# Kernel optimization log

Hardware: AMD Instinct MI355X
Metric: run time of the kernel (lower is better)

## Reference

```python
import jax, jax.numpy as jnp
import numpy as np

HEADS = 8
WSZ = 8
DIM_KEY = 32
DIM_VALUE = 32
DIM = 256
EPS = 1e-5


def setup_inputs() -> dict:
    key = jax.random.key(0)
    ks = jax.random.split(key, 8)
    B, C, H, W = 16, DIM, 128, 128
    inner_k = DIM_KEY * HEADS
    inner_v = DIM_VALUE * HEADS
    x = jax.random.normal(ks[0], (B, C, H, W), dtype=jnp.float32)
    g = jnp.ones((C,), dtype=jnp.float32)
    b = jnp.zeros((C,), dtype=jnp.float32)
    wq = jax.random.normal(ks[1], (inner_k, C), dtype=jnp.float32) * (C ** -0.5)
    wk = jax.random.normal(ks[2], (inner_k, C), dtype=jnp.float32) * (C ** -0.5)
    wv = jax.random.normal(ks[3], (inner_v, C), dtype=jnp.float32) * (C ** -0.5)
    local_w = jax.random.normal(ks[4], (inner_v, inner_v, 3, 3), dtype=jnp.float32) * ((inner_v * 9) ** -0.5)
    local_b = jnp.zeros((inner_v,), dtype=jnp.float32)
    out_w = jax.random.normal(ks[5], (C, inner_v), dtype=jnp.float32) * (inner_v ** -0.5)
    out_b = jnp.zeros((C,), dtype=jnp.float32)
    return {"x": x, "g": g, "b": b, "wq": wq, "wk": wk, "wv": wv,
            "local_w": local_w, "local_b": local_b, "out_w": out_w, "out_b": out_b}


def _to_windows(t, heads, wsz):
    # [B, heads*d, H, W] -> [B*X*Y, heads, wsz*wsz, d]
    B, Ch, H, W = t.shape
    d = Ch // heads
    X, Y = H // wsz, W // wsz
    t = t.reshape(B, heads, d, X, wsz, Y, wsz)
    t = t.transpose(0, 3, 5, 1, 4, 6, 2)  # B X Y heads w1 w2 d
    return t.reshape(B * X * Y, heads, wsz * wsz, d)


def _from_windows(t, B, heads, wsz, H, W):
    X, Y = H // wsz, W // wsz
    d = t.shape[-1]
    t = t.reshape(B, X, Y, heads, wsz, wsz, d)
    t = t.transpose(0, 3, 6, 1, 4, 2, 5)  # B heads d X w1 Y w2
    return t.reshape(B, heads * d, H, W)


def reference(x, g, b, wq, wk, wv, local_w, local_b, out_w, out_b):
    B, C, H, W = x.shape
    # ChanLayerNorm over channel dim (biased var)
    mean = jnp.mean(x, axis=1, keepdims=True)
    var = jnp.var(x, axis=1, keepdims=True)
    xn = (x - mean) / jnp.sqrt(var + EPS) * g[None, :, None, None] + b[None, :, None, None]
    # 1x1 conv projections as einsum
    q = jnp.einsum('oc,bchw->bohw', wq, xn)
    k = jnp.einsum('oc,bchw->bohw', wk, xn)
    v = jnp.einsum('oc,bchw->bohw', wv, xn)
    # local interactive 3x3 conv on v
    local_out = jax.lax.conv_general_dilated(
        v, local_w, window_strides=(1, 1), padding='SAME',
        dimension_numbers=('NCHW', 'OIHW', 'NCHW')) + local_b[None, :, None, None]
    # windowed attention
    qw = _to_windows(q, HEADS, WSZ)
    kw = _to_windows(k, HEADS, WSZ)
    vw = _to_windows(v, HEADS, WSZ)
    scale = DIM_KEY ** -0.5
    dots = jnp.einsum('whid,whjd->whij', qw, kw) * scale
    attn = jax.nn.softmax(dots, axis=-1)
    out = jnp.einsum('whij,whjd->whid', attn, vw)
    out = _from_windows(out, B, HEADS, WSZ, H, W)
    out = out + local_out
    # to_out 1x1 conv with bias
    return jnp.einsum('oc,bchw->bohw', out_w, out) + out_b[None, :, None, None]
```

## Files before the change

kernel.cpp:

```cpp
#include <hip/hip_runtime.h>

typedef __attribute__((ext_vector_type(8))) short short8;
typedef __attribute__((ext_vector_type(4))) float f32x4;
typedef __attribute__((ext_vector_type(2))) _Float16 h2;
typedef __attribute__((ext_vector_type(8))) _Float16 h8;

#define DEV static __device__ __forceinline__

typedef __attribute__((address_space(1))) void GVoid;
typedef __attribute__((address_space(3))) void LVoid;

DEV unsigned short f2h(float f) {
  _Float16 h = (_Float16)f;
  return __builtin_bit_cast(unsigned short, h);
}
DEV float h2f(unsigned short u) {
  return (float)__builtin_bit_cast(_Float16, u);
}
DEV unsigned pkh(float a, float b) {
  h2 h;
  h.x = (_Float16)a;
  h.y = (_Float16)b;
  return __builtin_bit_cast(unsigned, h);
}
DEV void cp16(void* lds_uniform_base, const void* gsrc) {
  __builtin_amdgcn_global_load_lds((GVoid*)gsrc, (LVoid*)lds_uniform_base, 16, 0, 0);
}
DEV float fdot2(h2 a, h2 b, float c) {
  return __builtin_amdgcn_fdot2(a, b, c, false);
}

DEV void xcd_remap(int& mb, int& nb) {
  const int gx = gridDim.x;
  const int p = blockIdx.x + gx * blockIdx.y;
  const int nwg = gx * gridDim.y;
  const int q = nwg >> 3;
  const int L = (p & 7) * q + (p >> 3);
  mb = L % gx;
  nb = L / gx;
}

__global__ __launch_bounds__(256) void setup_kernel(
    const float* __restrict__ wq, const float* __restrict__ wk, const float* __restrict__ wv,
    const float* __restrict__ lw, const float* __restrict__ ow,
    unsigned short* __restrict__ wqkvb, unsigned short* __restrict__ w2b,
    unsigned short* __restrict__ woutb, unsigned short* __restrict__ zp)
{
  int i = blockIdx.x * 256 + threadIdx.x;
  if (i < 196608) {
    float f = (i < 65536) ? wq[i] : (i < 131072) ? wk[i - 65536] : wv[i - 131072];
    wqkvb[i] = f2h(f);
  } else if (i < 786432) {
    int j = i - 196608;
    int co = j / 2304;
    int r = j - co * 2304;
    int tap = r >> 8;
    int ci = r & 255;
    w2b[j] = f2h(lw[(co * 256 + ci) * 9 + tap]);
  } else if (i < 851968) {
    int j = i - 786432;
    woutb[j] = f2h(ow[j]);
  } else if (i < 852096) {
    zp[i - 851968] = 0;
  }
}

__global__ __launch_bounds__(256) void ln_kernel(
    const float* __restrict__ x, const float* __restrict__ gw,
    const float* __restrict__ bw, unsigned short* __restrict__ xn)
{
  const int t = threadIdx.x;
  const int p = blockIdx.x * 256 + t;
  const int b = p >> 14;
  const int pix = p & 16383;
  const int h = pix >> 7;
  const int w = pix & 127;
  const float* xp = x + ((size_t)b << 22) + pix;

  float sum = 0.f, ss = 0.f;
#pragma unroll 8
  for (int c = 0; c < 256; ++c) {
    float f = xp[(size_t)c << 14];
    sum += f;
    ss += f * f;
  }
  float mean = sum * (1.f / 256.f);
  float var = ss * (1.f / 256.f) - mean * mean;
  float inv = rsqrtf(var + 1e-5f);

  const int pw = ((b * 16 + (h >> 3)) * 16 + (w >> 3)) * 64 + (h & 7) * 8 + (w & 7);
  unsigned short* op = xn + (size_t)pw * 256;
#pragma unroll 2
  for (int c = 0; c < 256; c += 4) {
    float f0 = xp[(size_t)(c + 0) << 14];
    float f1 = xp[(size_t)(c + 1) << 14];
    float f2 = xp[(size_t)(c + 2) << 14];
    float f3 = xp[(size_t)(c + 3) << 14];
    float v0 = (f0 - mean) * inv * gw[c + 0] + bw[c + 0];
    float v1 = (f1 - mean) * inv * gw[c + 1] + bw[c + 1];
    float v2 = (f2 - mean) * inv * gw[c + 2] + bw[c + 2];
    float v3 = (f3 - mean) * inv * gw[c + 3] + bw[c + 3];
    unsigned long long pk = (unsigned long long)pkh(v0, v1) |
                            ((unsigned long long)pkh(v2, v3) << 32);
    *(unsigned long long*)(op + c) = pk;
  }
}

DEV void mfma_tile(const unsigned short* As, const unsigned short* Bs,
                   int wm, int wn, int l15, int quad, f32x4 (&acc)[4][4])
{
  const int sx = l15 & 7;
#pragma unroll
  for (int ks = 0; ks < 2; ++ks) {
    const int sl = ((ks * 4 + quad) ^ sx) * 8;
    short8 a[4], b[4];
#pragma unroll
    for (int i = 0; i < 4; ++i)
      a[i] = *(const short8*)(As + (wm + i * 16 + l15) * 64 + sl);
#pragma unroll
    for (int j = 0; j < 4; ++j)
      b[j] = *(const short8*)(Bs + (wn + j * 16 + l15) * 64 + sl);
#pragma unroll
    for (int i = 0; i < 4; ++i)
#pragma unroll
      for (int j = 0; j < 4; ++j)
        acc[i][j] = __builtin_amdgcn_mfma_f32_16x16x32_f16(
            __builtin_bit_cast(h8, a[i]), __builtin_bit_cast(h8, b[j]), acc[i][j], 0, 0, 0);
  }
}

__global__ __launch_bounds__(256) void qkv_gemm(
    const unsigned short* __restrict__ wqkvb, const unsigned short* __restrict__ xn,
    unsigned short* __restrict__ qb, unsigned short* __restrict__ kb,
    unsigned short* __restrict__ vb)
{
  __shared__ __align__(16) unsigned short As[128 * 64];
  __shared__ __align__(16) unsigned short Bs[128 * 64];
  const int tid = threadIdx.x;
  const int lane = tid & 63;
  const int wave = tid >> 6;
  const int l15 = lane & 15;
  const int quad = lane >> 4;
  const int wm = (wave >> 1) * 64;
  const int wn = (wave & 1) * 64;
  const int sub = tid & 7;
  const int row0 = tid >> 3;
  const int ssub = sub ^ (row0 & 7);
  int mb, nb;
  xcd_remap(mb, nb);
  const int m0 = mb * 128;
  const int n0 = nb * 128;

  f32x4 acc[4][4];
  f32x4 zero = {0.f, 0.f, 0.f, 0.f};
#pragma unroll
  for (int i = 0; i < 4; ++i)
#pragma unroll
    for (int j = 0; j < 4; ++j) acc[i][j] = zero;

  for (int kt = 0; kt < 4; ++kt) {
    const int k0 = kt * 64;
#pragma unroll
    for (int it = 0; it < 4; ++it) {
      const int row = it * 32 + row0;
      cp16(As + (size_t)(it * 256 + wave * 64) * 8,
           wqkvb + (size_t)(m0 + row) * 256 + k0 + ssub * 8);
      cp16(Bs + (size_t)(it * 256 + wave * 64) * 8,
           xn + (size_t)(n0 + row) * 256 + k0 + ssub * 8);
    }
    __syncthreads();
    mfma_tile(As, Bs, wm, wn, l15, quad, acc);
    __syncthreads();
  }

  unsigned short* ob = (m0 < 256) ? qb : (m0 < 512) ? kb : vb;
  const int chb = (m0 & 255) + wm;
#pragma unroll
  for (int i = 0; i < 4; ++i) {
    const int ch = chb + i * 16 + quad * 4;
#pragma unroll
    for (int j = 0; j < 4; ++j) {
      const int n = n0 + wn + j * 16 + l15;
      unsigned long long pk = (unsigned long long)pkh(acc[i][j][0], acc[i][j][1]) |
                              ((unsigned long long)pkh(acc[i][j][2], acc[i][j][3]) << 32);
      *(unsigned long long*)(ob + (size_t)n * 256 + ch) = pk;
    }
  }
}

__global__ __launch_bounds__(128) void attn_kernel(
    const unsigned short* __restrict__ qb, const unsigned short* __restrict__ kb,
    const unsigned short* __restrict__ vb, unsigned short* __restrict__ attnb)
{
  __shared__ __align__(16) _Float16 ks2[2][64][40];
  __shared__ __align__(16) _Float16 vs2[2][32][64];
  const int tid = threadIdx.x;
  const int tok = tid & 63;
  const int hs = tid >> 6;
  const int win = blockIdx.x >> 2;
  const int head = (blockIdx.x & 3) * 2 + hs;
  const size_t base = (size_t)(win * 64 + tok) * 256 + head * 32;

  h2 q2[16];
  {
    const uint4* qp4 = (const uint4*)(qb + base);
    const uint4* kp4 = (const uint4*)(kb + base);
    const uint4* vp4 = (const uint4*)(vb + base);
    const _Float16 sc = (_Float16)0.17677669529663688f;
    h2 sc2;
    sc2.x = sc;
    sc2.y = sc;
#pragma unroll
    for (int i = 0; i < 4; ++i) {
      uint4 u = qp4[i];
      q2[i * 4 + 0] = __builtin_bit_cast(h2, u.x) * sc2;
      q2[i * 4 + 1] = __builtin_bit_cast(h2, u.y) * sc2;
      q2[i * 4 + 2] = __builtin_bit_cast(h2, u.z) * sc2;
      q2[i * 4 + 3] = __builtin_bit_cast(h2, u.w) * sc2;
      *(uint4*)&ks2[hs][tok][8 * i] = kp4[i];
      uint4 v = vp4[i];
      unsigned vv[4] = {v.x, v.y, v.z, v.w};
#pragma unroll
      for (int w = 0; w < 4; ++w) {
        h2 hv = __builtin_bit_cast(h2, vv[w]);
        int c = 2 * (i * 4 + w);
        vs2[hs][c + 0][tok] = hv.x;
        vs2[hs][c + 1][tok] = hv.y;
      }
    }
  }
  __syncthreads();

  float dots[64];
#pragma unroll
  for (int j = 0; j < 64; ++j) {
    const uint4* kr = (const uint4*)ks2[hs][j];
    float d = 0.f;
#pragma unroll
    for (int qq = 0; qq < 4; ++qq) {
      uint4 raw = kr[qq];
      d = fdot2(q2[4 * qq + 0], __builtin_bit_cast(h2, raw.x), d);
      d = fdot2(q2[4 * qq + 1], __builtin_bit_cast(h2, raw.y), d);
      d = fdot2(q2[4 * qq + 2], __builtin_bit_cast(h2, raw.z), d);
      d = fdot2(q2[4 * qq + 3], __builtin_bit_cast(h2, raw.w), d);
    }
    dots[j] = d;
  }
  float mx = -1e30f;
#pragma unroll
  for (int j = 0; j < 64; ++j) mx = fmaxf(mx, dots[j]);
  float s = 0.f;
#pragma unroll
  for (int j = 0; j < 64; ++j) {
    float e = __expf(dots[j] - mx);
    dots[j] = e;
    s += e;
  }
  const float rs = 1.f / s;

  h2 p2[32];
#pragma unroll
  for (int jp = 0; jp < 32; ++jp) {
    h2 p;
    p.x = (_Float16)dots[2 * jp];
    p.y = (_Float16)dots[2 * jp + 1];
    p2[jp] = p;
  }

  float of[32];
#pragma unroll
  for (int c = 0; c < 32; ++c) {
    const uint4* vr = (const uint4*)vs2[hs][c];
    float o = 0.f;
#pragma unroll
    for (int qq = 0; qq < 8; ++qq) {
      uint4 raw = vr[qq];
      o = fdot2(p2[4 * qq + 0], __builtin_bit_cast(h2, raw.x), o);
      o = fdot2(p2[4 * qq + 1], __builtin_bit_cast(h2, raw.y), o);
      o = fdot2(p2[4 * qq + 2], __builtin_bit_cast(h2, raw.z), o);
      o = fdot2(p2[4 * qq + 3], __builtin_bit_cast(h2, raw.w), o);
    }
    of[c] = o;
  }

  uint4* op4 = (uint4*)(attnb + base);
#pragma unroll
  for (int i = 0; i < 4; ++i) {
    uint4 o;
    o.x = pkh(of[8 * i + 0] * rs, of[8 * i + 1] * rs);
    o.y = pkh(of[8 * i + 2] * rs, of[8 * i + 3] * rs);
    o.z = pkh(of[8 * i + 4] * rs, of[8 * i + 5] * rs);
    o.w = pkh(of[8 * i + 6] * rs, of[8 * i + 7] * rs);
    op4[i] = o;
  }
}

__global__ __launch_bounds__(256) void conv_gemm(
    const unsigned short* __restrict__ w2b, const unsigned short* __restrict__ vbuf,
    const unsigned short* __restrict__ attnb, const float* __restrict__ lbias,
    const unsigned short* __restrict__ zp, unsigned short* __restrict__ sumb)
{
  __shared__ __align__(16) unsigned short As[128 * 64];
  __shared__ __align__(16) unsigned short Bs[128 * 64];
  const int tid = threadIdx.x;
  const int lane = tid & 63;
  const int wave = tid >> 6;
  const int l15 = lane & 15;
  const int quad = lane >> 4;
  const int wm = (wave >> 1) * 64;
  const int wn = (wave & 1) * 64;
  const int sub = tid & 7;
  const int row0 = tid >> 3;
  const int ssub = sub ^ (row0 & 7);
  int mb, nb;
  xcd_remap(mb, nb);
  const int m0 = mb * 128;
  const int n0 = nb * 128;

  int bi[4], hh[4], ww[4];
#pragma unroll
  for (int it = 0; it < 4; ++it) {
    int n = n0 + it * 32 + row0;
    int b = n >> 14;
    int r = n & 16383;
    int Xw = r >> 10;
    int r2 = r & 1023;
    int Yw = r2 >> 6;
    int t2 = r2 & 63;
    bi[it] = b;
    hh[it] = Xw * 8 + (t2 >> 3);
    ww[it] = Yw * 8 + (t2 & 7);
  }

  f32x4 acc[4][4];
  f32x4 zero = {0.f, 0.f, 0.f, 0.f};
#pragma unroll
  for (int i = 0; i < 4; ++i)
#pragma unroll
    for (int j = 0; j < 4; ++j) acc[i][j] = zero;

  for (int tap = 0; tap < 9; ++tap) {
    const int dy = tap / 3 - 1;
    const int dx = tap - (tap / 3) * 3 - 1;
    const unsigned short* bp[4];
    int bstep[4];
#pragma unroll
    for (int it = 0; it < 4; ++it) {
      int h2_ = hh[it] + dy, w2_ = ww[it] + dx;
      bool ok = ((unsigned)h2_ < 128u) && ((unsigned)w2_ < 128u);
      int nn = ((bi[it] * 16 + (h2_ >> 3)) * 16 + (w2_ >> 3)) * 64 + (h2_ & 7) * 8 + (w2_ & 7);
      bp[it] = ok ? (vbuf + (size_t)nn * 256 + ssub * 8) : (zp + ssub * 8);
      bstep[it] = ok ? 64 : 0;
    }
    for (int cc = 0; cc < 4; ++cc) {
#pragma unroll
      for (int it = 0; it < 4; ++it) {
        cp16(As + (size_t)(it * 256 + wave * 64) * 8,
             w2b + ((size_t)(m0 + it * 32 + row0) * 9 + tap) * 256 + cc * 64 + ssub * 8);
        cp16(Bs + (size_t)(it * 256 + wave * 64) * 8, bp[it] + cc * bstep[it]);
      }
      __syncthreads();
      mfma_tile(As, Bs, wm, wn, l15, quad, acc);
      __syncthreads();
    }
  }

#pragma unroll
  for (int i = 0; i < 4; ++i) {
    const int ch = m0 + wm + i * 16 + quad * 4;
    const float b0 = lbias[ch + 0], b1 = lbias[ch + 1], b2 = lbias[ch + 2], b3 = lbias[ch + 3];
#pragma unroll
    for (int j = 0; j < 4; ++j) {
      const int n = n0 + wn + j * 16 + l15;
      const unsigned* ap = (const unsigned*)(attnb + (size_t)n * 256 + ch);
      unsigned a0 = ap[0], a1 = ap[1];
      float r0 = acc[i][j][0] + b0 + h2f((unsigned short)(a0 & 0xffff));
      float r1 = acc[i][j][1] + b1 + h2f((unsigned short)(a0 >> 16));
      float r2 = acc[i][j][2] + b2 + h2f((unsigned short)(a1 & 0xffff));
      float r3 = acc[i][j][3] + b3 + h2f((unsigned short)(a1 >> 16));
      unsigned long long pk = (unsigned long long)pkh(r0, r1) |
                              ((unsigned long long)pkh(r2, r3) << 32);
      *(unsigned long long*)(sumb + (size_t)n * 256 + ch) = pk;
    }
  }
}

__global__ __launch_bounds__(256) void out_gemm(
    const unsigned short* __restrict__ woutb, const unsigned short* __restrict__ sumb,
    const float* __restrict__ obias, float* __restrict__ out)
{
  __shared__ __align__(16) unsigned short As[128 * 64];
  __shared__ __align__(16) unsigned short Bs[128 * 64];
  const int tid = threadIdx.x;
  const int lane = tid & 63;
  const int wave = tid >> 6;
  const int l15 = lane & 15;
  const int quad = lane >> 4;
  const int wm = (wave >> 1) * 64;
  const int wn = (wave & 1) * 64;
  const int sub = tid & 7;
  const int row0 = tid >> 3;
  const int ssub = sub ^ (row0 & 7);
  int mb, nb;
  xcd_remap(mb, nb);
  const int m0 = mb * 128;
  const int n0 = nb * 128;

  f32x4 acc[4][4];
  f32x4 zero = {0.f, 0.f, 0.f, 0.f};
#pragma unroll
  for (int i = 0; i < 4; ++i)
#pragma unroll
    for (int j = 0; j < 4; ++j) acc[i][j] = zero;

  for (int kt = 0; kt < 4; ++kt) {
    const int k0 = kt * 64;
#pragma unroll
    for (int it = 0; it < 4; ++it) {
      const int row = it * 32 + row0;
      cp16(As + (size_t)(it * 256 + wave * 64) * 8,
           woutb + (size_t)(m0 + row) * 256 + k0 + ssub * 8);
      cp16(Bs + (size_t)(it * 256 + wave * 64) * 8,
           sumb + (size_t)(n0 + row) * 256 + k0 + ssub * 8);
    }
    __syncthreads();
    mfma_tile(As, Bs, wm, wn, l15, quad, acc);
    __syncthreads();
  }

  int bb4[4], hw4[4];
#pragma unroll
  for (int j = 0; j < 4; ++j) {
    int n = n0 + wn + j * 16 + l15;
    int b = n >> 14;
    int r = n & 16383;
    int Xw = r >> 10;
    int r2 = r & 1023;
    int Yw = r2 >> 6;
    int t2 = r2 & 63;
    bb4[j] = b;
    hw4[j] = (Xw * 8 + (t2 >> 3)) * 128 + Yw * 8 + (t2 & 7);
  }
#pragma unroll
  for (int i = 0; i < 4; ++i) {
    const int mb2 = m0 + wm + i * 16 + quad * 4;
    const float o0 = obias[mb2 + 0], o1 = obias[mb2 + 1], o2 = obias[mb2 + 2], o3 = obias[mb2 + 3];
#pragma unroll
    for (int j = 0; j < 4; ++j) {
      float* o = out + ((size_t)(bb4[j] * 256 + mb2) << 14) + hw4[j];
      o[0] = acc[i][j][0] + o0;
      o[(size_t)1 << 14] = acc[i][j][1] + o1;
      o[(size_t)2 << 14] = acc[i][j][2] + o2;
      o[(size_t)3 << 14] = acc[i][j][3] + o3;
    }
  }
}

extern "C" void kernel_launch(void* const* d_in, const int* in_sizes, int n_in,
                              void* d_out, int out_size, void* d_ws, size_t ws_size,
                              hipStream_t stream)
{
  const float* x  = (const float*)d_in[0];
  const float* g  = (const float*)d_in[1];
  const float* bb = (const float*)d_in[2];
  const float* wq = (const float*)d_in[3];
  const float* wk = (const float*)d_in[4];
  const float* wv = (const float*)d_in[5];
  const float* lw = (const float*)d_in[6];
  const float* lb = (const float*)d_in[7];
  const float* ow = (const float*)d_in[8];
  const float* ob = (const float*)d_in[9];
  float* out = (float*)d_out;

  char* ws = (char*)d_ws;
  unsigned short* wqkvb = (unsigned short*)(ws + 0);
  unsigned short* w2b   = (unsigned short*)(ws + 393216);
  unsigned short* woutb = (unsigned short*)(ws + 1572864);
  unsigned short* zp    = (unsigned short*)(ws + 1703936);
  const size_t BUF0 = 1704192;

  int nimg = 16;
  while (nimg > 1 && BUF0 + 4ull * (size_t)nimg * 8388608ull > ws_size) nimg >>= 1;
  const size_t bufB = (size_t)nimg * 8388608ull;
  unsigned short* xnb = (unsigned short*)(ws + BUF0);
  unsigned short* qb  = (unsigned short*)(ws + BUF0 + bufB);
  unsigned short* kb  = (unsigned short*)(ws + BUF0 + 2 * bufB);
  unsigned short* vb  = (unsigned short*)(ws + BUF0 + 3 * bufB);
  unsigned short* attnb = xnb;
  unsigned short* sumb  = qb;

  setup_kernel<<<3329, 256, 0, stream>>>(wq, wk, wv, lw, ow, wqkvb, w2b, woutb, zp);

  const int nchunk = 16 / nimg;
  const int Nc = nimg * 16384;
  for (int c = 0; c < nchunk; ++c) {
    const float* xc = x + (size_t)c * nimg * 256 * 16384;
    float* oc = out + (size_t)c * nimg * 256 * 16384;
    ln_kernel<<<Nc / 256, 256, 0, stream>>>(xc, g, bb, xnb);
    qkv_gemm<<<dim3(6, Nc / 128), 256, 0, stream>>>(wqkvb, xnb, qb, kb, vb);
    attn_kernel<<<(Nc / 64) * 4, 128, 0, stream>>>(qb, kb, vb, attnb);
    conv_gemm<<<dim3(2, Nc / 128), 256, 0, stream>>>(w2b, vb, attnb, lb, zp, sumb);
    out_gemm<<<dim3(2, Nc / 128), 256, 0, stream>>>(woutb, sumb, ob, oc);
  }
}
```

Baseline: 1.497 ms.

## Double-buffer LDS tiles in qkv, conv and output GEMM kernels

Adds a second LDS buffer for the A and B tiles in the three GEMM kernels. The next k-slice is issued into the spare buffer before the MFMA work on the current slice, so global-to-LDS copies overlap with compute, and each iteration needs one barrier instead of two. The conv kernel's nested tap/channel loops are flattened into 36 steps so the prefetch can cross tap boundaries. This doubles LDS use per block to 64 KB, which may lower occupancy. The overlap also depends on whether cp16 is an asynchronous copy and on how the compiler places the waits.

```diff
diff --git a/kernel.cpp b/kernel.cpp
--- a/kernel.cpp
+++ b/kernel.cpp
@@ -134,8 +134,8 @@
     unsigned short* __restrict__ qb, unsigned short* __restrict__ kb,
     unsigned short* __restrict__ vb)
 {
-  __shared__ __align__(16) unsigned short As[128 * 64];
-  __shared__ __align__(16) unsigned short Bs[128 * 64];
+  __shared__ __align__(16) unsigned short As[2][128 * 64];
+  __shared__ __align__(16) unsigned short Bs[2][128 * 64];
   const int tid = threadIdx.x;
   const int lane = tid & 63;
   const int wave = tid >> 6;
@@ -158,19 +158,26 @@
 #pragma unroll
     for (int j = 0; j < 4; ++j) acc[i][j] = zero;
 
-  for (int kt = 0; kt < 4; ++kt) {
+  auto stage = [&](int kt, int d) {
     const int k0 = kt * 64;
 #pragma unroll
     for (int it = 0; it < 4; ++it) {
       const int row = it * 32 + row0;
-      cp16(As + (size_t)(it * 256 + wave * 64) * 8,
+      cp16(As[d] + (size_t)(it * 256 + wave * 64) * 8,
            wqkvb + (size_t)(m0 + row) * 256 + k0 + ssub * 8);
-      cp16(Bs + (size_t)(it * 256 + wave * 64) * 8,
+      cp16(Bs[d] + (size_t)(it * 256 + wave * 64) * 8,
            xn + (size_t)(n0 + row) * 256 + k0 + ssub * 8);
     }
+  };
+
+  stage(0, 0);
+  __syncthreads();
+  int cur = 0;
+  for (int kt = 0; kt < 4; ++kt) {
+    if (kt + 1 < 4) stage(kt + 1, cur ^ 1);
+    mfma_tile(As[cur], Bs[cur], wm, wn, l15, quad, acc);
     __syncthreads();
-    mfma_tile(As, Bs, wm, wn, l15, quad, acc);
-    __syncthreads();
+    cur ^= 1;
   }
 
   unsigned short* ob = (m0 < 256) ? qb : (m0 < 512) ? kb : vb;
@@ -300,8 +307,8 @@
     const unsigned short* __restrict__ attnb, const float* __restrict__ lbias,
     const unsigned short* __restrict__ zp, unsigned short* __restrict__ sumb)
 {
-  __shared__ __align__(16) unsigned short As[128 * 64];
-  __shared__ __align__(16) unsigned short Bs[128 * 64];
+  __shared__ __align__(16) unsigned short As[2][128 * 64];
+  __shared__ __align__(16) unsigned short Bs[2][128 * 64];
   const int tid = threadIdx.x;
   const int lane = tid & 63;
   const int wave = tid >> 6;
@@ -339,11 +346,11 @@
 #pragma unroll
     for (int j = 0; j < 4; ++j) acc[i][j] = zero;
 
-  for (int tap = 0; tap < 9; ++tap) {
+  const unsigned short* bp[4];
+  int bstep[4];
+  auto comp_bp = [&](int tap) {
     const int dy = tap / 3 - 1;
     const int dx = tap - (tap / 3) * 3 - 1;
-    const unsigned short* bp[4];
-    int bstep[4];
 #pragma unroll
     for (int it = 0; it < 4; ++it) {
       int h2_ = hh[it] + dy, w2_ = ww[it] + dx;
@@ -352,17 +359,29 @@
       bp[it] = ok ? (vbuf + (size_t)nn * 256 + ssub * 8) : (zp + ssub * 8);
       bstep[it] = ok ? 64 : 0;
     }
-    for (int cc = 0; cc < 4; ++cc) {
-#pragma unroll
-      for (int it = 0; it < 4; ++it) {
-        cp16(As + (size_t)(it * 256 + wave * 64) * 8,
-             w2b + ((size_t)(m0 + it * 32 + row0) * 9 + tap) * 256 + cc * 64 + ssub * 8);
-        cp16(Bs + (size_t)(it * 256 + wave * 64) * 8, bp[it] + cc * bstep[it]);
-      }
-      __syncthreads();
-      mfma_tile(As, Bs, wm, wn, l15, quad, acc);
-      __syncthreads();
-    }
+  };
+  auto stage = [&](int tap, int cc, int d) {
+#pragma unroll
+    for (int it = 0; it < 4; ++it) {
+      cp16(As[d] + (size_t)(it * 256 + wave * 64) * 8,
+           w2b + ((size_t)(m0 + it * 32 + row0) * 9 + tap) * 256 + cc * 64 + ssub * 8);
+      cp16(Bs[d] + (size_t)(it * 256 + wave * 64) * 8, bp[it] + cc * bstep[it]);
+    }
+  };
+
+  comp_bp(0);
+  stage(0, 0, 0);
+  __syncthreads();
+  int cur = 0;
+  for (int kk = 0; kk < 36; ++kk) {
+    const int nk = kk + 1;
+    if (nk < 36) {
+      if ((nk & 3) == 0) comp_bp(nk >> 2);
+      stage(nk >> 2, nk & 3, cur ^ 1);
+    }
+    mfma_tile(As[cur], Bs[cur], wm, wn, l15, quad, acc);
+    __syncthreads();
+    cur ^= 1;
   }
 
 #pragma unroll
@@ -389,8 +408,8 @@
     const unsigned short* __restrict__ woutb, const unsigned short* __restrict__ sumb,
     const float* __restrict__ obias, float* __restrict__ out)
 {
-  __shared__ __align__(16) unsigned short As[128 * 64];
-  __shared__ __align__(16) unsigned short Bs[128 * 64];
+  __shared__ __align__(16) unsigned short As[2][128 * 64];
+  __shared__ __align__(16) unsigned short Bs[2][128 * 64];
   const int tid = threadIdx.x;
   const int lane = tid & 63;
   const int wave = tid >> 6;
@@ -413,19 +432,26 @@
 #pragma unroll
     for (int j = 0; j < 4; ++j) acc[i][j] = zero;
 
-  for (int kt = 0; kt < 4; ++kt) {
+  auto stage = [&](int kt, int d) {
     const int k0 = kt * 64;
 #pragma unroll
     for (int it = 0; it < 4; ++it) {
       const int row = it * 32 + row0;
-      cp16(As + (size_t)(it * 256 + wave * 64) * 8,
+      cp16(As[d] + (size_t)(it * 256 + wave * 64) * 8,
            woutb + (size_t)(m0 + row) * 256 + k0 + ssub * 8);
-      cp16(Bs + (size_t)(it * 256 + wave * 64) * 8,
+      cp16(Bs[d] + (size_t)(it * 256 + wave * 64) * 8,
            sumb + (size_t)(n0 + row) * 256 + k0 + ssub * 8);
     }
+  };
+
+  stage(0, 0);
+  __syncthreads();
+  int cur = 0;
+  for (int kt = 0; kt < 4; ++kt) {
+    if (kt + 1 < 4) stage(kt + 1, cur ^ 1);
+    mfma_tile(As[cur], Bs[cur], wm, wn, l15, quad, acc);
     __syncthreads();
-    mfma_tile(As, Bs, wm, wn, l15, quad, acc);
-    __syncthreads();
+    cur ^= 1;
   }
 
   int bb4[4], hw4[4];
```

Result: slower. 1.566 ms (+4.6%).

## Widen GEMM M-tile to 256 and cache LN input in registers

Applied to the files above, without the earlier changes.

The three GEMM kernels (qkv, conv, out) now use a 256x128 block tile, so each block covers all 256 output channels and the activation tile is loaded once instead of twice. This removes the redundant B-tile loads and halves the grid. Separately, the layernorm kernel keeps the input channels in registers as packed fp16 during the statistics pass, so x is read from global memory once instead of twice. Risks are higher register pressure (32 accumulators per lane, a 128-entry register array), lower occupancy, larger LDS use, and the input being rounded to fp16 before normalization.

```diff
diff --git a/kernel.cpp b/kernel.cpp
--- a/kernel.cpp
+++ b/kernel.cpp
@@ -77,12 +77,18 @@
   const int w = pix & 127;
   const float* xp = x + ((size_t)b << 22) + pix;
 
+  h2 xr[128];
   float sum = 0.f, ss = 0.f;
-#pragma unroll 8
-  for (int c = 0; c < 256; ++c) {
-    float f = xp[(size_t)c << 14];
-    sum += f;
-    ss += f * f;
+#pragma unroll
+  for (int i = 0; i < 128; ++i) {
+    float f0 = xp[(size_t)(2 * i + 0) << 14];
+    float f1 = xp[(size_t)(2 * i + 1) << 14];
+    sum += f0 + f1;
+    ss += f0 * f0 + f1 * f1;
+    h2 pk;
+    pk.x = (_Float16)f0;
+    pk.y = (_Float16)f1;
+    xr[i] = pk;
   }
   float mean = sum * (1.f / 256.f);
   float var = ss * (1.f / 256.f) - mean * mean;
@@ -90,38 +96,36 @@
 
   const int pw = ((b * 16 + (h >> 3)) * 16 + (w >> 3)) * 64 + (h & 7) * 8 + (w & 7);
   unsigned short* op = xn + (size_t)pw * 256;
-#pragma unroll 2
-  for (int c = 0; c < 256; c += 4) {
-    float f0 = xp[(size_t)(c + 0) << 14];
-    float f1 = xp[(size_t)(c + 1) << 14];
-    float f2 = xp[(size_t)(c + 2) << 14];
-    float f3 = xp[(size_t)(c + 3) << 14];
-    float v0 = (f0 - mean) * inv * gw[c + 0] + bw[c + 0];
-    float v1 = (f1 - mean) * inv * gw[c + 1] + bw[c + 1];
-    float v2 = (f2 - mean) * inv * gw[c + 2] + bw[c + 2];
-    float v3 = (f3 - mean) * inv * gw[c + 3] + bw[c + 3];
+#pragma unroll
+  for (int i = 0; i < 64; ++i) {
+    h2 a = xr[2 * i], c = xr[2 * i + 1];
+    const int ch = 4 * i;
+    float v0 = ((float)a.x - mean) * inv * gw[ch + 0] + bw[ch + 0];
+    float v1 = ((float)a.y - mean) * inv * gw[ch + 1] + bw[ch + 1];
+    float v2 = ((float)c.x - mean) * inv * gw[ch + 2] + bw[ch + 2];
+    float v3 = ((float)c.y - mean) * inv * gw[ch + 3] + bw[ch + 3];
     unsigned long long pk = (unsigned long long)pkh(v0, v1) |
                             ((unsigned long long)pkh(v2, v3) << 32);
-    *(unsigned long long*)(op + c) = pk;
-  }
-}
-
-DEV void mfma_tile(const unsigned short* As, const unsigned short* Bs,
-                   int wm, int wn, int l15, int quad, f32x4 (&acc)[4][4])
+    *(unsigned long long*)(op + ch) = pk;
+  }
+}
+
+DEV void mfma_tile256(const unsigned short* As, const unsigned short* Bs,
+                      int wm, int wn, int l15, int quad, f32x4 (&acc)[8][4])
 {
   const int sx = l15 & 7;
 #pragma unroll
   for (int ks = 0; ks < 2; ++ks) {
     const int sl = ((ks * 4 + quad) ^ sx) * 8;
-    short8 a[4], b[4];
-#pragma unroll
-    for (int i = 0; i < 4; ++i)
+    short8 a[8], b[4];
+#pragma unroll
+    for (int i = 0; i < 8; ++i)
       a[i] = *(const short8*)(As + (wm + i * 16 + l15) * 64 + sl);
 #pragma unroll
     for (int j = 0; j < 4; ++j)
       b[j] = *(const short8*)(Bs + (wn + j * 16 + l15) * 64 + sl);
 #pragma unroll
-    for (int i = 0; i < 4; ++i)
+    for (int i = 0; i < 8; ++i)
 #pragma unroll
       for (int j = 0; j < 4; ++j)
         acc[i][j] = __builtin_amdgcn_mfma_f32_16x16x32_f16(
@@ -134,50 +138,51 @@
     unsigned short* __restrict__ qb, unsigned short* __restrict__ kb,
     unsigned short* __restrict__ vb)
 {
-  __shared__ __align__(16) unsigned short As[128 * 64];
+  __shared__ __align__(16) unsigned short As[256 * 64];
   __shared__ __align__(16) unsigned short Bs[128 * 64];
   const int tid = threadIdx.x;
   const int lane = tid & 63;
   const int wave = tid >> 6;
   const int l15 = lane & 15;
   const int quad = lane >> 4;
-  const int wm = (wave >> 1) * 64;
+  const int wm = (wave >> 1) * 128;
   const int wn = (wave & 1) * 64;
   const int sub = tid & 7;
   const int row0 = tid >> 3;
   const int ssub = sub ^ (row0 & 7);
   int mb, nb;
   xcd_remap(mb, nb);
-  const int m0 = mb * 128;
+  const int m0 = mb * 256;
   const int n0 = nb * 128;
 
-  f32x4 acc[4][4];
+  f32x4 acc[8][4];
   f32x4 zero = {0.f, 0.f, 0.f, 0.f};
 #pragma unroll
-  for (int i = 0; i < 4; ++i)
+  for (int i = 0; i < 8; ++i)
 #pragma unroll
     for (int j = 0; j < 4; ++j) acc[i][j] = zero;
 
   for (int kt = 0; kt < 4; ++kt) {
     const int k0 = kt * 64;
 #pragma unroll
+    for (int it = 0; it < 8; ++it) {
+      cp16(As + (size_t)(it * 256 + wave * 64) * 8,
+           wqkvb + (size_t)(m0 + it * 32 + row0) * 256 + k0 + ssub * 8);
+    }
+#pragma unroll
     for (int it = 0; it < 4; ++it) {
-      const int row = it * 32 + row0;
-      cp16(As + (size_t)(it * 256 + wave * 64) * 8,
-           wqkvb + (size_t)(m0 + row) * 256 + k0 + ssub * 8);
       cp16(Bs + (size_t)(it * 256 + wave * 64) * 8,
-           xn + (size_t)(n0 + row) * 256 + k0 + ssub * 8);
+           xn + (size_t)(n0 + it * 32 + row0) * 256 + k0 + ssub * 8);
     }
     __syncthreads();
-    mfma_tile(As, Bs, wm, wn, l15, quad, acc);
+    mfma_tile256(As, Bs, wm, wn, l15, quad, acc);
     __syncthreads();
   }
 
   unsigned short* ob = (m0 < 256) ? qb : (m0 < 512) ? kb : vb;
-  const int chb = (m0 & 255) + wm;
-#pragma unroll
-  for (int i = 0; i < 4; ++i) {
-    const int ch = chb + i * 16 + quad * 4;
+#pragma unroll
+  for (int i = 0; i < 8; ++i) {
+    const int ch = wm + i * 16 + quad * 4;
 #pragma unroll
     for (int j = 0; j < 4; ++j) {
       const int n = n0 + wn + j * 16 + l15;
@@ -300,21 +305,20 @@
     const unsigned short* __restrict__ attnb, const float* __restrict__ lbias,
     const unsigned short* __restrict__ zp, unsigned short* __restrict__ sumb)
 {
-  __shared__ __align__(16) unsigned short As[128 * 64];
+  __shared__ __align__(16) unsigned short As[256 * 64];
   __shared__ __align__(16) unsigned short Bs[128 * 64];
   const int tid = threadIdx.x;
   const int lane = tid & 63;
   const int wave = tid >> 6;
   const int l15 = lane & 15;
   const int quad = lane >> 4;
-  const int wm = (wave >> 1) * 64;
+  const int wm = (wave >> 1) * 128;
   const int wn = (wave & 1) * 64;
   const int sub = tid & 7;
   const int row0 = tid >> 3;
   const int ssub = sub ^ (row0 & 7);
   int mb, nb;
   xcd_remap(mb, nb);
-  const int m0 = mb * 128;
   const int n0 = nb * 128;
 
   int bi[4], hh[4], ww[4];
@@ -332,10 +336,10 @@
     ww[it] = Yw * 8 + (t2 & 7);
   }
 
-  f32x4 acc[4][4];
+  f32x4 acc[8][4];
   f32x4 zero = {0.f, 0.f, 0.f, 0.f};
 #pragma unroll
-  for (int i = 0; i < 4; ++i)
+  for (int i = 0; i < 8; ++i)
 #pragma unroll
     for (int j = 0; j < 4; ++j) acc[i][j] = zero;
 
@@ -354,20 +358,23 @@
     }
     for (int cc = 0; cc < 4; ++cc) {
 #pragma unroll
+      for (int it = 0; it < 8; ++it) {
+        cp16(As + (size_t)(it * 256 + wave * 64) * 8,
+             w2b + ((size_t)(it * 32 + row0) * 9 + tap) * 256 + cc * 64 + ssub * 8);
+      }
+#pragma unroll
       for (int it = 0; it < 4; ++it) {
-        cp16(As + (size_t)(it * 256 + wave * 64) * 8,
-             w2b + ((size_t)(m0 + it * 32 + row0) * 9 + tap) * 256 + cc * 64 + ssub * 8);
         cp16(Bs + (size_t)(it * 256 + wave * 64) * 8, bp[it] + cc * bstep[it]);
       }
       __syncthreads();
-      mfma_tile(As, Bs, wm, wn, l15, quad, acc);
+      mfma_tile256(As, Bs, wm, wn, l15, quad, acc);
       __syncthreads();
     }
   }
 
 #pragma unroll
-  for (int i = 0; i < 4; ++i) {
-    const int ch = m0 + wm + i * 16 + quad * 4;
+  for (int i = 0; i < 8; ++i) {
+    const int ch = wm + i * 16 + quad * 4;
     const float b0 = lbias[ch + 0], b1 = lbias[ch + 1], b2 = lbias[ch + 2], b3 = lbias[ch + 3];
 #pragma unroll
     for (int j = 0; j < 4; ++j) {
@@ -389,42 +396,43 @@
     const unsigned short* __restrict__ woutb, const unsigned short* __restrict__ sumb,
     const float* __restrict__ obias, float* __restrict__ out)
 {
-  __shared__ __align__(16) unsigned short As[128 * 64];
+  __shared__ __align__(16) unsigned short As[256 * 64];
   __shared__ __align__(16) unsigned short Bs[128 * 64];
   const int tid = threadIdx.x;
   const int lane = tid & 63;
   const int wave = tid >> 6;
   const int l15 = lane & 15;
   const int quad = lane >> 4;
-  const int wm = (wave >> 1) * 64;
+  const int wm = (wave >> 1) * 128;
   const int wn = (wave & 1) * 64;
   const int sub = tid & 7;
   const int row0 = tid >> 3;
   const int ssub = sub ^ (row0 & 7);
   int mb, nb;
   xcd_remap(mb, nb);
-  const int m0 = mb * 128;
   const int n0 = nb * 128;
 
-  f32x4 acc[4][4];
+  f32x4 acc[8][4];
   f32x4 zero = {0.f, 0.f, 0.f, 0.f};
 #pragma unroll
-  for (int i = 0; i < 4; ++i)
+  for (int i = 0; i < 8; ++i)
 #pragma unroll
     for (int j = 0; j < 4; ++j) acc[i][j] = zero;
 
   for (int kt = 0; kt < 4; ++kt) {
     const int k0 = kt * 64;
 #pragma unroll
+    for (int it = 0; it < 8; ++it) {
+      cp16(As + (size_t)(it * 256 + wave * 64) * 8,
+           woutb + (size_t)(it * 32 + row0) * 256 + k0 + ssub * 8);
+    }
+#pragma unroll
     for (int it = 0; it < 4; ++it) {
-      const int row = it * 32 + row0;
-      cp16(As + (size_t)(it * 256 + wave * 64) * 8,
-           woutb + (size_t)(m0 + row) * 256 + k0 + ssub * 8);
       cp16(Bs + (size_t)(it * 256 + wave * 64) * 8,
-           sumb + (size_t)(n0 + row) * 256 + k0 + ssub * 8);
+           sumb + (size_t)(n0 + it * 32 + row0) * 256 + k0 + ssub * 8);
     }
     __syncthreads();
-    mfma_tile(As, Bs, wm, wn, l15, quad, acc);
+    mfma_tile256(As, Bs, wm, wn, l15, quad, acc);
     __syncthreads();
   }
 
@@ -442,8 +450,8 @@
     hw4[j] = (Xw * 8 + (t2 >> 3)) * 128 + Yw * 8 + (t2 & 7);
   }
 #pragma unroll
-  for (int i = 0; i < 4; ++i) {
-    const int mb2 = m0 + wm + i * 16 + quad * 4;
+  for (int i = 0; i < 8; ++i) {
+    const int mb2 = wm + i * 16 + quad * 4;
     const float o0 = obias[mb2 + 0], o1 = obias[mb2 + 1], o2 = obias[mb2 + 2], o3 = obias[mb2 + 3];
 #pragma unroll
     for (int j = 0; j < 4; ++j) {
@@ -497,9 +505,9 @@
     const float* xc = x + (size_t)c * nimg * 256 * 16384;
     float* oc = out + (size_t)c * nimg * 256 * 16384;
     ln_kernel<<<Nc / 256, 256, 0, stream>>>(xc, g, bb, xnb);
-    qkv_gemm<<<dim3(6, Nc / 128), 256, 0, stream>>>(wqkvb, xnb, qb, kb, vb);
+    qkv_gemm<<<dim3(3, Nc / 128), 256, 0, stream>>>(wqkvb, xnb, qb, kb, vb);
     attn_kernel<<<(Nc / 64) * 4, 128, 0, stream>>>(qb, kb, vb, attnb);
-    conv_gemm<<<dim3(2, Nc / 128), 256, 0, stream>>>(w2b, vb, attnb, lb, zp, sumb);
-    out_gemm<<<dim3(2, Nc / 128), 256, 0, stream>>>(woutb, sumb, ob, oc);
-  }
-}
+    conv_gemm<<<dim3(1, Nc / 128), 256, 0, stream>>>(w2b, vb, attnb, lb, zp, sumb);
+    out_gemm<<<dim3(1, Nc / 128), 256, 0, stream>>>(woutb, sumb, ob, oc);
+  }
+}
```

Result: slower. 1.579 ms (+5.4%).
